# Performance work log

Measured on AMD Instinct MI355X. Metric: run time of the kernel, lower is better.

## Reference

```python
import jax, jax.numpy as jnp
import numpy as np

DIM = 1024
H = 16
DPH = DIM // H  # 64
B, S = 4, 2048


def setup_inputs() -> dict:
    key = jax.random.key(0)
    ks = jax.random.split(key, 9)
    s_in = 1.0 / np.sqrt(DIM)
    s_out = 1.0 / np.sqrt(H * DPH)
    return {
        "x": jax.random.normal(ks[0], (B, S, DIM), dtype=jnp.float32),
        "Wq": jax.random.normal(ks[1], (H, DIM, DPH), dtype=jnp.float32) * s_in,
        "bq": jax.random.normal(ks[2], (H, DPH), dtype=jnp.float32) * 0.01,
        "Wk": jax.random.normal(ks[3], (DIM, DPH), dtype=jnp.float32) * s_in,
        "bk": jax.random.normal(ks[4], (DPH,), dtype=jnp.float32) * 0.01,
        "Wv": jax.random.normal(ks[5], (DIM, DPH), dtype=jnp.float32) * s_in,
        "bv": jax.random.normal(ks[6], (DPH,), dtype=jnp.float32) * 0.01,
        "Wo": jax.random.normal(ks[7], (H * DPH, DIM), dtype=jnp.float32) * s_out,
        "bo": jax.random.normal(ks[8], (DIM,), dtype=jnp.float32) * 0.01,
    }


def reference(x, Wq, bq, Wk, bk, Wv, bv, Wo, bo):
    # Multi-query attention: per-head Q, shared K/V. dropout p=0 -> identity.
    scale = 1.0 / jnp.sqrt(jnp.asarray(DPH, dtype=jnp.float32))
    q = jnp.einsum("bsd,hde->bhse", x, Wq) + bq[None, :, None, :]  # [B,H,S,dph]
    k = jnp.einsum("bsd,de->bse", x, Wk) + bk                      # [B,S,dph]
    v = jnp.einsum("bsd,de->bse", x, Wv) + bv                      # [B,S,dph]
    scores = jnp.einsum("bhse,bte->bhst", q, k) * scale            # [B,H,S,S]
    attn = jax.nn.softmax(scores, axis=-1)
    o = jnp.einsum("bhst,bte->bhse", attn, v)                      # [B,H,S,dph]
    # concat heads in head order along last dim -> [B,S,H*dph]
    o = jnp.transpose(o, (0, 2, 1, 3)).reshape(B, S, H * DPH)
    return jnp.einsum("bsf,fd->bsd", o, Wo) + bo
```

## Files before the change

kernel.cpp:

```cpp
#include <hip/hip_runtime.h>
#include <hip/hip_bf16.h>
#include <hip/hip_fp16.h>


typedef _Float16 f16x8 __attribute__((ext_vector_type(8)));
typedef _Float16 f16x4 __attribute__((ext_vector_type(4)));
typedef _Float16 f16x2 __attribute__((ext_vector_type(2)));
typedef float f32x4 __attribute__((ext_vector_type(4)));
typedef float f32x16 __attribute__((ext_vector_type(16)));

#define MFMA16(a, b, c) __builtin_amdgcn_mfma_f32_16x16x32_f16((a), (b), (c), 0, 0, 0)
#define MFMA32(a, b, c) __builtin_amdgcn_mfma_f32_32x32x16_f16((a), (b), (c), 0, 0, 0)
#define PKRTZ(a, b) __builtin_bit_cast(f16x2, __builtin_amdgcn_cvt_pkrtz((a), (b)))

__device__ __forceinline__ void gll16(const void* g, void* l) {
  __builtin_amdgcn_global_load_lds(
      (__attribute__((address_space(1))) void*)const_cast<void*>(g),
      (__attribute__((address_space(3))) void*)l, 16, 0, 0);
}

__global__ __launch_bounds__(256) void pack_all_kernel(
    const float* __restrict__ x, const float* __restrict__ Wq,
    const float* __restrict__ Wk, const float* __restrict__ Wv,
    const float* __restrict__ Wo,
    _Float16* __restrict__ xh, _Float16* __restrict__ wqkvT,
    _Float16* __restrict__ woT) {
  int bid = blockIdx.x;
  if (bid < 4096) {
    int i = bid * 256 + threadIdx.x;
    const float4* s = (const float4*)x + (size_t)i * 2;
    float4 a = s[0], b = s[1];
    f16x8 h;
    h[0] = (_Float16)a.x; h[1] = (_Float16)a.y; h[2] = (_Float16)a.z; h[3] = (_Float16)a.w;
    h[4] = (_Float16)b.x; h[5] = (_Float16)b.y; h[6] = (_Float16)b.z; h[7] = (_Float16)b.w;
    ((f16x8*)xh)[i] = h;
    return;
  }
  int i = (bid - 4096) * 256 + threadIdx.x;
  if (i < 1048576) {
    int n = i >> 10, d = i & 1023;
    int h = n >> 6, e = n & 63;
    wqkvT[i] = (_Float16)Wq[h * 65536 + d * 64 + e];
  } else if (i < 1114112) {
    int j = i - 1048576;
    int e = j >> 10, d = j & 1023;
    wqkvT[i] = (_Float16)Wk[d * 64 + e];
  } else if (i < 1179648) {
    int j = i - 1114112;
    int e = j >> 10, d = j & 1023;
    wqkvT[i] = (_Float16)Wv[d * 64 + e];
  } else {
    int j = i - 1179648;
    int d = j >> 10, f = j & 1023;
    woT[j] = (_Float16)Wo[f * 1024 + d];
  }
}

struct GemmAcc {
  f32x4 acc[4][4];
};

__device__ __forceinline__ void gemm128_core(
    const _Float16* __restrict__ A, const _Float16* __restrict__ Bp,
    int m0, int n0, _Float16* abuf, _Float16* bbuf, GemmAcc& g) {
  const int tid = threadIdx.x;
  const int lane = tid & 63, wave = tid >> 6;
  const int wr = wave >> 1, wc = wave & 1;
  const int g4 = lane >> 4, l15 = lane & 15;

  const char* Ag = (const char*)(A + (size_t)m0 * 1024);
  const char* Bg = (const char*)(Bp + (size_t)n0 * 1024);

  const int c0 = tid, c1 = tid + 256;
  const size_t aoff0 = (size_t)(c0 >> 2) * 2048 + (size_t)(c0 & 3) * 16;
  const size_t aoff1 = (size_t)(c1 >> 2) * 2048 + (size_t)(c1 & 3) * 16;
  char* ldsa0 = (char*)abuf + c0 * 16;
  char* ldsa1 = (char*)abuf + c1 * 16;
  char* ldsb0 = (char*)bbuf + c0 * 16;
  char* ldsb1 = (char*)bbuf + c1 * 16;

  const char* ar[4];
  const char* br[4];
  #pragma unroll
  for (int mt = 0; mt < 4; mt++)
    ar[mt] = (const char*)abuf + ((wr << 6) + (mt << 4) + l15) * 64 + (g4 << 4);
  #pragma unroll
  for (int nt = 0; nt < 4; nt++)
    br[nt] = (const char*)bbuf + ((wc << 6) + (nt << 4) + l15) * 64 + (g4 << 4);

  for (int k0 = 0; k0 < 1024; k0 += 32) {
    const size_t kb = (size_t)k0 * 2;
    gll16(Ag + aoff0 + kb, ldsa0);
    gll16(Ag + aoff1 + kb, ldsa1);
    gll16(Bg + aoff0 + kb, ldsb0);
    gll16(Bg + aoff1 + kb, ldsb1);
    __syncthreads();
    f16x8 af[4], bf[4];
    #pragma unroll
    for (int mt = 0; mt < 4; mt++) af[mt] = *(const f16x8*)ar[mt];
    #pragma unroll
    for (int nt = 0; nt < 4; nt++) bf[nt] = *(const f16x8*)br[nt];
    #pragma unroll
    for (int mt = 0; mt < 4; mt++)
      #pragma unroll
      for (int nt = 0; nt < 4; nt++)
        g.acc[mt][nt] = MFMA16(af[mt], bf[nt], g.acc[mt][nt]);
    __syncthreads();
  }
}

__global__ __launch_bounds__(256) void gemm_qkv_kernel(
    const _Float16* __restrict__ xh, const _Float16* __restrict__ wT,
    const float* __restrict__ bq, const float* __restrict__ bk,
    const float* __restrict__ bv,
    _Float16* __restrict__ qh, _Float16* __restrict__ kh,
    _Float16* __restrict__ vth) {
  __shared__ __align__(16) _Float16 abuf[128 * 32];
  __shared__ __align__(16) _Float16 bbuf[128 * 32];
  const int lane = threadIdx.x & 63, wave = threadIdx.x >> 6;
  const int wr = wave >> 1, wc = wave & 1;
  const int g4 = lane >> 4, l15 = lane & 15;
  const int m0 = blockIdx.x * 128;
  const int n0 = blockIdx.y * 128;
  GemmAcc g = {};
  gemm128_core(xh, wT, m0, n0, abuf, bbuf, g);

  const float QSCALE = 0.18033688011112042f;
  #pragma unroll
  for (int mt = 0; mt < 4; mt++) {
    int rbase = m0 + wr * 64 + mt * 16 + (g4 << 2);
    int bb = rbase >> 11;
    int s = rbase & 2047;
    #pragma unroll
    for (int nt = 0; nt < 4; nt++) {
      int n = n0 + wc * 64 + nt * 16 + l15;
      if (n < 1024) {
        float bias = bq[n];
        int h = n >> 6, e = n & 63;
        _Float16* dst = qh + (((size_t)(bb * 16 + h) * 2048 + s) * 64 + e);
        #pragma unroll
        for (int r = 0; r < 4; r++)
          dst[(size_t)r * 64] = (_Float16)((g.acc[mt][nt][r] + bias) * QSCALE);
      } else if (n < 1088) {
        int e = n - 1024;
        float bias = bk[e];
        _Float16* dst = kh + ((size_t)bb * 2048 + s) * 64 + e;
        #pragma unroll
        for (int r = 0; r < 4; r++) dst[(size_t)r * 64] = (_Float16)(g.acc[mt][nt][r] + bias);
      } else {
        int e = n - 1088;
        float bias = bv[e];
        f16x4 t;
        #pragma unroll
        for (int r = 0; r < 4; r++) t[r] = (_Float16)(g.acc[mt][nt][r] + bias);
        *(f16x4*)(vth + ((size_t)bb * 64 + e) * 2048 + s) = t;
      }
    }
  }
}

__global__ __launch_bounds__(256) void gemm_out_kernel(
    const _Float16* __restrict__ oh, const _Float16* __restrict__ woT,
    const float* __restrict__ bo, float* __restrict__ out) {
  __shared__ __align__(16) _Float16 abuf[128 * 32];
  __shared__ __align__(16) _Float16 bbuf[128 * 32];
  const int lane = threadIdx.x & 63, wave = threadIdx.x >> 6;
  const int wr = wave >> 1, wc = wave & 1;
  const int g4 = lane >> 4, l15 = lane & 15;
  const int m0 = blockIdx.x * 128;
  const int n0 = blockIdx.y * 128;
  GemmAcc g = {};
  gemm128_core(oh, woT, m0, n0, abuf, bbuf, g);

  #pragma unroll
  for (int mt = 0; mt < 4; mt++) {
    int rbase = m0 + wr * 64 + mt * 16 + (g4 << 2);
    #pragma unroll
    for (int nt = 0; nt < 4; nt++) {
      int n = n0 + wc * 64 + nt * 16 + l15;
      float bias = bo[n];
      #pragma unroll
      for (int r = 0; r < 4; r++)
        out[(size_t)(rbase + r) * 1024 + n] = g.acc[mt][nt][r] + bias;
    }
  }
}

__global__ __launch_bounds__(1024) void attn_kernel(
    const _Float16* __restrict__ qh, const _Float16* __restrict__ kh,
    const _Float16* __restrict__ vth, _Float16* __restrict__ oh) {
  __shared__ __align__(16) _Float16 smem[32768];
  const int tid = threadIdx.x;
  const int lane = tid & 63, wave = tid >> 6;
  const int l31 = lane & 31, h = lane >> 5;
  const int b = blockIdx.z, hd = blockIdx.y;
  const int q0 = blockIdx.x * 512;

  const _Float16* Qrow = qh + (((size_t)(b * 16 + hd) * 2048 + q0 + wave * 32 + l31) * 64);
  f16x8 qf[4];
  #pragma unroll
  for (int s = 0; s < 4; s++) qf[s] = *(const f16x8*)(Qrow + s * 16 + h * 8);

  const char* Kb = (const char*)(kh + (size_t)b * 2048 * 64);
  const char* Vb = (const char*)(vth + (size_t)b * 64 * 2048);

  const bool isK = tid < 512;
  const char* src;
  int dstbase;
  {
    int c = isK ? tid : (tid - 512);
    int m = c >> 3, c8 = c & 7;
    int gc = c8 ^ (m & 7);
    if (isK) {
      int tsrc = (m & 51) | ((m & 4) << 1) | ((m & 8) >> 1);
      src = Kb + (size_t)tsrc * 128 + gc * 16;
      dstbase = c * 16;
    } else {
      src = Vb + (size_t)m * 4096 + gc * 16;
      dstbase = 16384 + c * 16;
    }
  }
  char* const ldsb = (char*)smem;
  const size_t srcstep = isK ? 8192 : 128;

  const int swz = l31 & 7;
  int ro[4][2];
  #pragma unroll
  for (int s = 0; s < 4; s++) {
    int ch = ((2 * s + h) ^ swz) << 4;
    ro[s][0] = l31 * 128 + ch;
    ro[s][1] = (l31 + 32) * 128 + ch;
  }

  float negm = 0.f, l_run = 0.f;
  f32x16 oa0 = {}, oa1 = {};
  const f16x2 one2 = {(_Float16)1.0f, (_Float16)1.0f};

  auto STAGE = [&](int t, int buf) {
    gll16(src + (size_t)t * srcstep, ldsb + buf * 8192 + dstbase);
  };

  STAGE(0, 0);
  __syncthreads();

  for (int it = 0; it < 32; ++it) {
    const int cur = it & 1;
    const char* kb = ldsb + cur * 8192;
    const char* vb = kb + 16384;

    if (it + 1 < 32) STAGE(it + 1, cur ^ 1);

    f32x16 s0, s1;
    #pragma unroll
    for (int i = 0; i < 16; i++) { s0[i] = negm; s1[i] = negm; }
    #pragma unroll
    for (int s = 0; s < 4; s++) {
      f16x8 a0 = *(const f16x8*)(kb + ro[s][0]);
      f16x8 a1 = *(const f16x8*)(kb + ro[s][1]);
      s0 = MFMA32(a0, qf[s], s0);
      s1 = MFMA32(a1, qf[s], s1);
    }

    float vm[8];
    #pragma unroll
    for (int i = 0; i < 8; i++)
      vm[i] = fmaxf(fmaxf(s0[i], s0[i + 8]), fmaxf(s1[i], s1[i + 8]));
    float pm = fmaxf(fmaxf(fmaxf(vm[0], vm[1]), fmaxf(vm[2], vm[3])),
                     fmaxf(fmaxf(vm[4], vm[5]), fmaxf(vm[6], vm[7])));
    pm = fmaxf(pm, __shfl_xor(pm, 32));

    if (__any(pm > 8.0f)) {
      float delta = fmaxf(pm, 0.f);
      float al = __builtin_amdgcn_exp2f(-delta);
      l_run *= al;
      oa0 *= al;
      oa1 *= al;
      negm -= delta;
      #pragma unroll
      for (int i = 0; i < 16; i++) { s0[i] -= delta; s1[i] -= delta; }
    }

    #pragma unroll
    for (int i = 0; i < 16; i++) {
      s0[i] = __builtin_amdgcn_exp2f(s0[i]);
      s1[i] = __builtin_amdgcn_exp2f(s1[i]);
    }

    f16x2 pp[16];
    #pragma unroll
    for (int j = 0; j < 8; j++) pp[j] = PKRTZ(s0[2 * j], s0[2 * j + 1]);
    #pragma unroll
    for (int j = 0; j < 8; j++) pp[8 + j] = PKRTZ(s1[2 * j], s1[2 * j + 1]);

    float ps0 = 0.f, ps1 = 0.f, ps2 = 0.f, ps3 = 0.f;
    #pragma unroll
    for (int j = 0; j < 4; j++) {
      ps0 = __builtin_amdgcn_fdot2(pp[j], one2, ps0, false);
      ps1 = __builtin_amdgcn_fdot2(pp[4 + j], one2, ps1, false);
      ps2 = __builtin_amdgcn_fdot2(pp[8 + j], one2, ps2, false);
      ps3 = __builtin_amdgcn_fdot2(pp[12 + j], one2, ps3, false);
    }
    l_run += (ps0 + ps1) + (ps2 + ps3);

    f16x8 pf[4];
    #pragma unroll
    for (int s = 0; s < 4; s++) {
      f16x4 lo = __builtin_shufflevector(pp[s * 4], pp[s * 4 + 1], 0, 1, 2, 3);
      f16x4 hi = __builtin_shufflevector(pp[s * 4 + 2], pp[s * 4 + 3], 0, 1, 2, 3);
      pf[s] = __builtin_shufflevector(lo, hi, 0, 1, 2, 3, 4, 5, 6, 7);
    }

    #pragma unroll
    for (int s = 0; s < 4; s++) {
      f16x8 v0 = *(const f16x8*)(vb + ro[s][0]);
      f16x8 v1 = *(const f16x8*)(vb + ro[s][1]);
      oa0 = MFMA32(v0, pf[s], oa0);
      oa1 = MFMA32(v1, pf[s], oa1);
    }

    __syncthreads();
  }

  l_run += __shfl_xor(l_run, 32);
  _Float16* ob = smem + wave * 2048;
  float invl = 1.0f / l_run;
  #pragma unroll
  for (int rh = 0; rh < 4; rh++) {
    f16x4 t0, t1;
    #pragma unroll
    for (int j = 0; j < 4; j++) {
      t0[j] = (_Float16)(oa0[rh * 4 + j] * invl);
      t1[j] = (_Float16)(oa1[rh * 4 + j] * invl);
    }
    *(f16x4*)&ob[l31 * 64 + ((rh ^ swz) * 8) + h * 4] = t0;
    *(f16x4*)&ob[l31 * 64 + (((rh + 4) ^ swz) * 8) + h * 4] = t1;
  }
  const int q_ = lane >> 1, hf = lane & 1;
  const size_t orow = ((size_t)b * 2048 + q0 + wave * 32 + q_) * 1024 + hd * 64 + hf * 32;
  #pragma unroll
  for (int c = 0; c < 4; c++) {
    f16x8 v = *(const f16x8*)&ob[q_ * 64 + (((hf * 4 + c) ^ (q_ & 7)) * 8)];
    *(f16x8*)(oh + orow + c * 8) = v;
  }
}

extern "C" void kernel_launch(void* const* d_in, const int* in_sizes, int n_in,
                              void* d_out, int out_size, void* d_ws, size_t ws_size,
                              hipStream_t stream) {
  const float* x  = (const float*)d_in[0];
  const float* Wq = (const float*)d_in[1];
  const float* bq = (const float*)d_in[2];
  const float* Wk = (const float*)d_in[3];
  const float* bk = (const float*)d_in[4];
  const float* Wv = (const float*)d_in[5];
  const float* bv = (const float*)d_in[6];
  const float* Wo = (const float*)d_in[7];
  const float* bo = (const float*)d_in[8];
  float* out = (float*)d_out;
  char* ws = (char*)d_ws;

  _Float16* xh   = (_Float16*)(ws);
  _Float16* wqkv = (_Float16*)(ws + 16777216);
  _Float16* woT  = (_Float16*)(ws + 19136512);
  _Float16* qh   = (_Float16*)(ws + 21233664);
  _Float16* kh   = (_Float16*)(ws + 38010880);
  _Float16* vth  = (_Float16*)(ws + 39059456);
  _Float16* oh   = (_Float16*)(ws + 40108032);

  pack_all_kernel<<<12800, 256, 0, stream>>>(x, Wq, Wk, Wv, Wo, xh, wqkv, woT);
  gemm_qkv_kernel<<<dim3(64, 9), 256, 0, stream>>>(xh, wqkv, bq, bk, bv, qh, kh, vth);
  attn_kernel<<<dim3(4, 16, 4), 1024, 0, stream>>>(qh, kh, vth, oh);
  gemm_out_kernel<<<dim3(64, 8), 256, 0, stream>>>(oh, woT, bo, out);
}
```

Measured before the change: 161.2 us.

## Double-buffer GEMM LDS staging, swizzle workgroup order, raise MFMA priority in attention

The shared GEMM core now double-buffers its LDS tiles, issuing the async global-to-LDS loads for the next K step before computing the current one, so load latency overlaps with MFMA work. Both GEMM kernels remap block indices with an XCD-style swizzle (groups of 8) so neighbouring tiles land on the same die and share L2. The attention kernel wraps its two MFMA phases in s_setprio to favour matrix issue across waves. Doubling LDS per block can reduce occupancy, and the swizzle assumes the grid size divides by 8.

```diff
diff --git a/kernel.cpp b/kernel.cpp
--- a/kernel.cpp
+++ b/kernel.cpp
@@ -74,32 +74,33 @@
   const int c0 = tid, c1 = tid + 256;
   const size_t aoff0 = (size_t)(c0 >> 2) * 2048 + (size_t)(c0 & 3) * 16;
   const size_t aoff1 = (size_t)(c1 >> 2) * 2048 + (size_t)(c1 & 3) * 16;
-  char* ldsa0 = (char*)abuf + c0 * 16;
-  char* ldsa1 = (char*)abuf + c1 * 16;
-  char* ldsb0 = (char*)bbuf + c0 * 16;
-  char* ldsb1 = (char*)bbuf + c1 * 16;
-
-  const char* ar[4];
-  const char* br[4];
-  #pragma unroll
-  for (int mt = 0; mt < 4; mt++)
-    ar[mt] = (const char*)abuf + ((wr << 6) + (mt << 4) + l15) * 64 + (g4 << 4);
-  #pragma unroll
-  for (int nt = 0; nt < 4; nt++)
-    br[nt] = (const char*)bbuf + ((wc << 6) + (nt << 4) + l15) * 64 + (g4 << 4);
-
-  for (int k0 = 0; k0 < 1024; k0 += 32) {
-    const size_t kb = (size_t)k0 * 2;
-    gll16(Ag + aoff0 + kb, ldsa0);
-    gll16(Ag + aoff1 + kb, ldsa1);
-    gll16(Bg + aoff0 + kb, ldsb0);
-    gll16(Bg + aoff1 + kb, ldsb1);
-    __syncthreads();
+
+  auto STAGE = [&](int kstep, int buf) {
+    const size_t kb = (size_t)kstep * 64;
+    char* la = (char*)abuf + buf * 8192;
+    char* lb = (char*)bbuf + buf * 8192;
+    gll16(Ag + aoff0 + kb, la + c0 * 16);
+    gll16(Ag + aoff1 + kb, la + c1 * 16);
+    gll16(Bg + aoff0 + kb, lb + c0 * 16);
+    gll16(Bg + aoff1 + kb, lb + c1 * 16);
+  };
+
+  const int arow = ((wr << 6) + l15) * 64 + (g4 << 4);
+  const int brow = ((wc << 6) + l15) * 64 + (g4 << 4);
+
+  STAGE(0, 0);
+  __syncthreads();
+
+  for (int k = 0; k < 32; k++) {
+    const int cur = k & 1;
+    if (k + 1 < 32) STAGE(k + 1, cur ^ 1);
+    const char* la = (const char*)abuf + cur * 8192;
+    const char* lb = (const char*)bbuf + cur * 8192;
     f16x8 af[4], bf[4];
     #pragma unroll
-    for (int mt = 0; mt < 4; mt++) af[mt] = *(const f16x8*)ar[mt];
-    #pragma unroll
-    for (int nt = 0; nt < 4; nt++) bf[nt] = *(const f16x8*)br[nt];
+    for (int mt = 0; mt < 4; mt++) af[mt] = *(const f16x8*)(la + arow + mt * 1024);
+    #pragma unroll
+    for (int nt = 0; nt < 4; nt++) bf[nt] = *(const f16x8*)(lb + brow + nt * 1024);
     #pragma unroll
     for (int mt = 0; mt < 4; mt++)
       #pragma unroll
@@ -115,15 +116,19 @@
     const float* __restrict__ bv,
     _Float16* __restrict__ qh, _Float16* __restrict__ kh,
     _Float16* __restrict__ vth) {
-  __shared__ __align__(16) _Float16 abuf[128 * 32];
-  __shared__ __align__(16) _Float16 bbuf[128 * 32];
+  __shared__ __align__(16) _Float16 abuf[2][128 * 32];
+  __shared__ __align__(16) _Float16 bbuf[2][128 * 32];
   const int lane = threadIdx.x & 63, wave = threadIdx.x >> 6;
   const int wr = wave >> 1, wc = wave & 1;
   const int g4 = lane >> 4, l15 = lane & 15;
-  const int m0 = blockIdx.x * 128;
-  const int n0 = blockIdx.y * 128;
+  const int nwg = gridDim.x * gridDim.y;
+  const int orig = blockIdx.y * gridDim.x + blockIdx.x;
+  const int cpx = nwg >> 3;
+  const int swzb = (orig & 7) * cpx + (orig >> 3);
+  const int m0 = (swzb % gridDim.x) * 128;
+  const int n0 = (swzb / gridDim.x) * 128;
   GemmAcc g = {};
-  gemm128_core(xh, wT, m0, n0, abuf, bbuf, g);
+  gemm128_core(xh, wT, m0, n0, abuf[0], bbuf[0], g);
 
   const float QSCALE = 0.18033688011112042f;
   #pragma unroll
@@ -162,15 +167,19 @@
 __global__ __launch_bounds__(256) void gemm_out_kernel(
     const _Float16* __restrict__ oh, const _Float16* __restrict__ woT,
     const float* __restrict__ bo, float* __restrict__ out) {
-  __shared__ __align__(16) _Float16 abuf[128 * 32];
-  __shared__ __align__(16) _Float16 bbuf[128 * 32];
+  __shared__ __align__(16) _Float16 abuf[2][128 * 32];
+  __shared__ __align__(16) _Float16 bbuf[2][128 * 32];
   const int lane = threadIdx.x & 63, wave = threadIdx.x >> 6;
   const int wr = wave >> 1, wc = wave & 1;
   const int g4 = lane >> 4, l15 = lane & 15;
-  const int m0 = blockIdx.x * 128;
-  const int n0 = blockIdx.y * 128;
+  const int nwg = gridDim.x * gridDim.y;
+  const int orig = blockIdx.y * gridDim.x + blockIdx.x;
+  const int cpx = nwg >> 3;
+  const int swzb = (orig & 7) * cpx + (orig >> 3);
+  const int m0 = (swzb % gridDim.x) * 128;
+  const int n0 = (swzb / gridDim.x) * 128;
   GemmAcc g = {};
-  gemm128_core(oh, woT, m0, n0, abuf, bbuf, g);
+  gemm128_core(oh, woT, m0, n0, abuf[0], bbuf[0], g);
 
   #pragma unroll
   for (int mt = 0; mt < 4; mt++) {
@@ -253,6 +262,7 @@
     f32x16 s0, s1;
     #pragma unroll
     for (int i = 0; i < 16; i++) { s0[i] = negm; s1[i] = negm; }
+    __builtin_amdgcn_s_setprio(1);
     #pragma unroll
     for (int s = 0; s < 4; s++) {
       f16x8 a0 = *(const f16x8*)(kb + ro[s][0]);
@@ -260,6 +270,7 @@
       s0 = MFMA32(a0, qf[s], s0);
       s1 = MFMA32(a1, qf[s], s1);
     }
+    __builtin_amdgcn_s_setprio(0);
 
     float vm[8];
     #pragma unroll
@@ -310,6 +321,7 @@
       pf[s] = __builtin_shufflevector(lo, hi, 0, 1, 2, 3, 4, 5, 6, 7);
     }
 
+    __builtin_amdgcn_s_setprio(1);
     #pragma unroll
     for (int s = 0; s < 4; s++) {
       f16x8 v0 = *(const f16x8*)(vb + ro[s][0]);
@@ -317,6 +329,7 @@
       oa0 = MFMA32(v0, pf[s], oa0);
       oa1 = MFMA32(v1, pf[s], oa1);
     }
+    __builtin_amdgcn_s_setprio(0);
 
     __syncthreads();
   }
```

After: 173.8 us. 1.08x slower.
